# Kernel optimization log

Hardware: AMD Instinct MI355X
Metric: run time of the kernel (lower is better)

Reference implementation:

```python
import jax, jax.numpy as jnp
import numpy as np

B, CHAN, HW = 256, 3, 32
NC, DIM = 10, 48
FC1_IN = (HW - 4) * (HW - 4) * 64 // 4  # 12544


def _signed_root(m, a, p, b):
    # sign(sign(m)+0.1) * ((|m|+a)^p - b)
    return jnp.sign(jnp.sign(m) + 0.1) * (jnp.power(jnp.abs(m) + a, p) - b)


def setup_inputs() -> dict:
    key = jax.random.key(0)
    ks = jax.random.split(key, 12)
    f32 = jnp.float32
    x = jax.random.normal(ks[0], (B, CHAN, HW, HW), f32)
    conv1_w = jax.random.normal(ks[1], (32, CHAN, 3, 3), f32) * (1.0 / np.sqrt(CHAN * 9))
    conv1_b = jax.random.normal(ks[2], (32,), f32) * 0.01
    conv2_w = jax.random.normal(ks[3], (64, 32, 3, 3), f32) * (1.0 / np.sqrt(32 * 9))
    conv2_b = jax.random.normal(ks[4], (64,), f32) * 0.01
    fc1_w = jax.random.normal(ks[5], (128, FC1_IN), f32) * (1.0 / np.sqrt(FC1_IN))
    fc1_b = jax.random.normal(ks[6], (128,), f32) * 0.01
    fc2_w = jax.random.normal(ks[7], (128, 128), f32) * (1.0 / np.sqrt(128))
    fc2_b = jax.random.normal(ks[8], (128,), f32) * 0.01
    fc3_w = jax.random.normal(ks[9], (DIM, 128), f32) * (1.0 / np.sqrt(128))
    fc3_b = jax.random.normal(ks[10], (DIM,), f32) * 0.01
    centers = jnp.eye(NC, DIM, dtype=f32)
    # GaussMoments constants: standard-normal joint moments (non-trainable)
    mom_weight = jnp.ones((DIM,), f32)          # order-1 moment weights, reused for all orders in source
    gm1 = jnp.zeros((DIM,), f32)                # E[z_i] = 0
    eye = jnp.eye(DIM, dtype=f32)
    gm2 = eye                                   # E[z_i z_j] = delta_ij
    gm3 = jnp.zeros((DIM, DIM, DIM), f32)       # odd moments vanish
    gm4 = (eye[:, :, None, None] * eye[None, None, :, :]
           + eye[:, None, :, None] * eye[None, :, None, :]
           + eye[:, None, None, :] * eye[None, :, :, None])  # Isserlis
    return {"x": x, "conv1_w": conv1_w, "conv1_b": conv1_b, "conv2_w": conv2_w,
            "conv2_b": conv2_b, "fc1_w": fc1_w, "fc1_b": fc1_b, "fc2_w": fc2_w,
            "fc2_b": fc2_b, "fc3_w": fc3_w, "fc3_b": fc3_b, "centers": centers,
            "mom_weight": mom_weight, "gm1": gm1, "gm2": gm2, "gm3": gm3, "gm4": gm4}


def _backbone(x, c1w, c1b, c2w, c2b, f1w, f1b, f2w, f2b, f3w, f3b):
    dn = ("NCHW", "OIHW", "NCHW")
    h = jax.lax.conv_general_dilated(x, c1w, (1, 1), "VALID", dimension_numbers=dn)
    h = jax.nn.relu(h + c1b[None, :, None, None])
    h = jax.lax.conv_general_dilated(h, c2w, (1, 1), "VALID", dimension_numbers=dn)
    h = jax.nn.relu(h + c2b[None, :, None, None])
    h = jax.lax.reduce_window(h, -jnp.inf, jax.lax.max, (1, 1, 2, 2), (1, 1, 2, 2), "VALID")
    h = h.reshape(h.shape[0], -1)
    h = jax.nn.relu(h @ f1w.T + f1b)
    h = jax.nn.relu(h @ f2w.T + f2b)
    return h @ f3w.T + f3b  # [B, DIM]


def _gmm_tail(z, centers, mom_weight, gm1, gm2, gm3, gm4):
    Bv, d, C = z.shape[0], DIM, NC
    diff = z[:, None, :] - centers[None, :, :]              # [B,C,d]
    dist_sq = jnp.sum(diff * diff, axis=-1)                 # [B,C]
    expo = -0.5 * dist_sq
    expo_safe = expo - jnp.max(expo, axis=1, keepdims=True)  # MaxPool1d(10) == max over classes
    numer_safe = jnp.exp(expo_safe)
    resp = numer_safe / jnp.sum(numer_safe, axis=1, keepdims=True)
    onehot = jax.nn.one_hot(jnp.argmin(dist_sq, axis=-1), C, dtype=diff.dtype)  # [B,C]
    do = diff * onehot[:, :, None]                          # [B,C,d]
    cw = jnp.sum(onehot, axis=0)                            # [C]
    eps = 1e-7
    m1 = jnp.sum(do, axis=0) / (cw[:, None] + eps)          # [C,d]
    pair = jnp.einsum("bci,bcj->bcij", do, do).reshape(Bv, C, d * d)  # [B,C,d^2]
    m2 = jnp.sum(pair, axis=0).reshape(C, d, d) / (cw[:, None, None] + eps)
    m3 = jnp.einsum("bcp,bck->cpk", pair, do).reshape(C, d, d, d)      # NOT count-normalized (as in source)
    m4 = jnp.einsum("bcp,bcq->cpq", pair, pair).reshape(C, d, d, d, d)  # NOT count-normalized (as in source)
    m2 = _signed_root(m2, 0.25, 0.5, 0.5)
    m3 = _signed_root(m3, 0.19245008973, 0.3333333333, 0.57735026919)
    m4 = _signed_root(m4, 0.15749013123, 0.25, 0.62996052494)
    t1 = gm1
    t2 = _signed_root(gm2, 0.25, 0.5, 0.5)
    t3 = _signed_root(gm3, 0.19245008973, 0.3333333333, 0.57735026919)
    t4 = _signed_root(gm4, 0.15749013123, 0.25, 0.62996052494)
    cwn = cw / jnp.sum(cw)
    # moment weights broadcast over the LAST axis only (torch repeat semantics in source)
    p1 = jnp.sum(cwn[:, None] * mom_weight * (m1 - t1[None]) ** 2)
    p2 = jnp.sum(cwn[:, None, None] * mom_weight * (m2 - t2[None]) ** 2)
    p3 = jnp.sum(cwn[:, None, None, None] * mom_weight * (m3 - t3[None]) ** 2)
    p4 = jnp.sum(cwn[:, None, None, None, None] * mom_weight * (m4 - t4[None]) ** 2)
    log_resp = jnp.log(jnp.clip(resp, 1e-8))
    return log_resp, p1, p2, p3, p4


def reference(x, conv1_w, conv1_b, conv2_w, conv2_b, fc1_w, fc1_b, fc2_w, fc2_b,
              fc3_w, fc3_b, centers, mom_weight, gm1, gm2, gm3, gm4):
    z = _backbone(x, conv1_w, conv1_b, conv2_w, conv2_b, fc1_w, fc1_b, fc2_w, fc2_b, fc3_w, fc3_b)
    return _gmm_tail(z, centers, mom_weight, gm1, gm2, gm3, gm4)
```

## Files before the change

### kernel.cpp

```cpp
#include <hip/hip_runtime.h>
#include <math.h>

#define BATCH   256
#define NCLS    10
#define DIM     48

#define OFF_H1B   0
#define OFF_PAIR  0
#define OFF_FC1P  602112
#define OFF_WT    2699264
#define OFF_PTBH  4500000
#define OFF_PTBL  5300000
#define OFF_POOL  7372800
#define OFF_DO    10596352
#define OFF_CW    10608640
#define OFF_INT   10608656
#define OFF_WPH   10612000
#define OFF_WPL   10622000

typedef __attribute__((ext_vector_type(8))) short short8;
typedef __attribute__((ext_vector_type(4))) float floatx4;
typedef unsigned short u16;
typedef unsigned int u32;

__device__ __forceinline__ u16 f2bf(float v) {
    u32 u = __float_as_uint(v);
    return (u16)((u + 0x7fffu + ((u >> 16) & 1u)) >> 16);
}
__device__ __forceinline__ float bf2f(u16 h) {
    return __uint_as_float(((u32)h) << 16);
}

__device__ __forceinline__ float sroot_half(float m) {
    float s = (m < 0.f) ? -1.f : 1.f;
    return s * (sqrtf(fabsf(m) + 0.25f) - 0.5f);
}
__device__ __forceinline__ float sroot_cbrt(float m) {
    float s = (m < 0.f) ? -1.f : 1.f;
    return s * (cbrtf(fabsf(m) + 0.19245008973f) - 0.57735026919f);
}
__device__ __forceinline__ float sroot_quarter(float m) {
    float s = (m < 0.f) ? -1.f : 1.f;
    return s * (sqrtf(sqrtf(fabsf(m) + 0.15749013123f)) - 0.62996052494f);
}

__global__ void k_conv1(const float* __restrict__ x, const float* __restrict__ w,
                        const float* __restrict__ bias, u16* __restrict__ h1b,
                        const float* __restrict__ c2w, u16* __restrict__ wph,
                        u16* __restrict__ wpl, float* __restrict__ cw,
                        int* __restrict__ cls_cnt, float* __restrict__ out) {
    int blk = blockIdx.x;
    int tid = threadIdx.x;
    if (blk == 900) {
        for (int i = tid; i < 18432; i += 256) {
            int icr = i & 7, rest = i >> 3;
            int oc = rest & 63, rest2 = rest >> 6;
            int icq = rest2 & 3, s = rest2 >> 2;
            int ic = icq * 8 + icr;
            float v = c2w[(oc * 32 + ic) * 9 + s];
            u16 hi = f2bf(v);
            wph[i] = hi;
            wpl[i] = f2bf(v - bf2f(hi));
        }
        return;
    }
    if (blk == 0) {
        if (tid < 16) { cw[tid] = 0.f; cls_cnt[tid] = 0; }
        else if (tid < 20) out[2560 + tid - 16] = 0.f;
    }
    int pos = blk * 256 + tid;
    int b = pos / 900, rem = pos % 900;
    int y = rem / 30, xx = rem % 30;
    float win[27];
#pragma unroll
    for (int ic = 0; ic < 3; ic++)
#pragma unroll
        for (int ky = 0; ky < 3; ky++)
#pragma unroll
            for (int kx = 0; kx < 3; kx++)
                win[ic * 9 + ky * 3 + kx] = x[b * 3072 + ic * 1024 + (y + ky) * 32 + xx + kx];
    u16* hp = h1b + (size_t)pos * 64;
#pragma unroll
    for (int ch = 0; ch < 4; ch++) {
        u32 hiw[4], low[4];
#pragma unroll
        for (int a2 = 0; a2 < 4; a2++) {
            u16 h2[2], l2[2];
#pragma unroll
            for (int e = 0; e < 2; e++) {
                int oc = ch * 8 + a2 * 2 + e;
                float s = bias[oc];
#pragma unroll
                for (int k = 0; k < 27; k++) s = fmaf(win[k], w[oc * 27 + k], s);
                s = fmaxf(s, 0.f);
                u16 hi = f2bf(s);
                h2[e] = hi;
                l2[e] = f2bf(s - bf2f(hi));
            }
            hiw[a2] = (u32)h2[0] | ((u32)h2[1] << 16);
            low[a2] = (u32)l2[0] | ((u32)l2[1] << 16);
        }
        *(uint4*)(hp + ch * 8)      = make_uint4(hiw[0], hiw[1], hiw[2], hiw[3]);
        *(uint4*)(hp + 32 + ch * 8) = make_uint4(low[0], low[1], low[2], low[3]);
    }
}

__global__ void k_conv2(const u16* __restrict__ h1b, const u16* __restrict__ wph,
                        const u16* __restrict__ wpl, const float* __restrict__ bias,
                        float* __restrict__ pooled) {
    __shared__ u16 hs[256 * 72];
    int blk = blockIdx.x;
    int b = blk >> 2, sub = blk & 3;
    int hy = sub >> 1, hx = sub & 1;
    int row0 = hy * 14, col0 = hx * 14;
    int tid = threadIdx.x;
    for (int i = tid; i < 2048; i += 256) {
        int p = i >> 3, c8 = i & 7;
        int r = p >> 4, cc = p & 15;
        size_t gp = (size_t)b * 900 + (size_t)(row0 + r) * 30 + col0 + cc;
        *(uint4*)(&hs[p * 72 + c8 * 8]) = *(const uint4*)(&h1b[gp * 64 + c8 * 8]);
    }
    int wv = tid >> 6, lane = tid & 63;
    int n = lane & 15, quad = lane >> 4;
    int ocb = wv * 16 + n;
    float bv = bias[ocb];
    short8 bh[9], bl[9];
#pragma unroll
    for (int s = 0; s < 9; s++) {
        int off = (((s * 4 + quad) * 64) + ocb) * 8;
        bh[s] = *(const short8*)(&wph[off]);
        bl[s] = *(const short8*)(&wpl[off]);
    }
    __syncthreads();
    int ml = lane & 15;
    for (int t = 0; t < 13; t++) {
        int gA = t * 4 + (ml >> 2);
        int d = ml & 3;
        int gc = (gA < 49) ? gA : 0;
        int py = gc / 7, px = gc % 7;
        int rb = 2 * py + (d >> 1), cb = 2 * px + (d & 1);
        floatx4 acc = {0.f, 0.f, 0.f, 0.f};
#pragma unroll
        for (int s = 0; s < 9; s++) {
            int ky = s / 3, kx = s % 3;
            int pos = (rb + ky) * 16 + cb + kx;
            short8 ah = *(const short8*)(&hs[pos * 72 + quad * 8]);
            short8 al = *(const short8*)(&hs[pos * 72 + 32 + quad * 8]);
            acc = __builtin_amdgcn_mfma_f32_16x16x32_bf16(ah, bh[s], acc, 0, 0, 0);
            acc = __builtin_amdgcn_mfma_f32_16x16x32_bf16(ah, bl[s], acc, 0, 0, 0);
            acc = __builtin_amdgcn_mfma_f32_16x16x32_bf16(al, bh[s], acc, 0, 0, 0);
        }
        int G = t * 4 + quad;
        if (G < 49) {
            float v = fmaxf(fmaxf(acc.x, acc.y), fmaxf(acc.z, acc.w));
            v = fmaxf(v + bv, 0.f);
            int pyg = hy * 7 + G / 7, pxg = hx * 7 + G % 7;
            pooled[(size_t)b * 12544 + ocb * 196 + pyg * 14 + pxg] = v;
        }
    }
}

__global__ void k_wtrans(const float* __restrict__ w, float* __restrict__ wT) {
    __shared__ float tile[32][33];
    int kb = blockIdx.x % 392, nb = blockIdx.x / 392;
    int tid = threadIdx.x;
    int tx = tid & 31, ty = tid >> 5;
    int k0 = kb * 32, n0 = nb * 32;
#pragma unroll
    for (int r = 0; r < 4; r++)
        tile[tx][ty * 4 + r] = w[(n0 + ty * 4 + r) * 12544 + k0 + tx];
    __syncthreads();
#pragma unroll
    for (int r = 0; r < 4; r++)
        wT[(k0 + ty * 4 + r) * 128 + n0 + tx] = tile[ty * 4 + r][tx];
}

__global__ void k_fc1(const float* __restrict__ pooled, const float* __restrict__ wT,
                      float* __restrict__ fc1p) {
    __shared__ __align__(16) float Alds[16 * 196];
    int blk = blockIdx.x;
    int sg = blk >> 6, kc = blk & 63;
    int tid = threadIdx.x;
    int m0 = sg * 16, k0 = kc * 196;
    for (int i = tid; i < 784; i += 256) {
        int m = i / 49, u = i % 49;
        ((float4*)Alds)[m * 49 + u] = ((const float4*)(pooled + (m0 + m) * 12544 + k0))[u];
    }
    __syncthreads();
    int n2 = tid & 63, mg = tid >> 6;
    const float* wp = wT + (size_t)k0 * 128 + n2;
    const float* arow = Alds + mg * 4 * 196;
    float acc[4][2];
#pragma unroll
    for (int j = 0; j < 4; j++) { acc[j][0] = 0.f; acc[j][1] = 0.f; }
    for (int k = 0; k < 196; k += 2) {
        float wa0 = wp[k * 128],        wb0 = wp[k * 128 + 64];
        float wa1 = wp[(k + 1) * 128],  wb1 = wp[(k + 1) * 128 + 64];
#pragma unroll
        for (int j = 0; j < 4; j++) {
            float2 av = *(const float2*)(arow + j * 196 + k);
            acc[j][0] = fmaf(av.x, wa0, acc[j][0]);
            acc[j][0] = fmaf(av.y, wa1, acc[j][0]);
            acc[j][1] = fmaf(av.x, wb0, acc[j][1]);
            acc[j][1] = fmaf(av.y, wb1, acc[j][1]);
        }
    }
#pragma unroll
    for (int j = 0; j < 4; j++) {
        int m = m0 + mg * 4 + j;
        fc1p[kc * 32768 + m * 128 + n2]      = acc[j][0];
        fc1p[kc * 32768 + m * 128 + n2 + 64] = acc[j][1];
    }
}

__global__ void k_fc23a(const float* __restrict__ fc1p, const float* __restrict__ f1b,
                        const float* __restrict__ w2, const float* __restrict__ b2,
                        const float* __restrict__ w3, const float* __restrict__ b3,
                        const float* __restrict__ centers, float* __restrict__ out,
                        float* __restrict__ dov, float* __restrict__ pairm,
                        float* __restrict__ cw, int* __restrict__ cls_cnt,
                        int* __restrict__ cls_idx) {
    __shared__ float a[128], h[128], zb[48], dvs[48];
    __shared__ float dist[10];
    __shared__ float smn, ssum;
    __shared__ int sarg;
    int b = blockIdx.x, t = threadIdx.x;
    float s0 = f1b[t];
    for (int p = 0; p < 64; p++) s0 += fc1p[p * 32768 + b * 128 + t];
    a[t] = fmaxf(s0, 0.f);
    __syncthreads();
    float s = b2[t];
    const float* wr = w2 + t * 128;
#pragma unroll 4
    for (int k = 0; k < 128; k++) s = fmaf(wr[k], a[k], s);
    h[t] = fmaxf(s, 0.f);
    __syncthreads();
    if (t < 48) {
        float s3 = b3[t];
        const float* wr3 = w3 + t * 128;
#pragma unroll 4
        for (int k = 0; k < 128; k++) s3 = fmaf(wr3[k], h[k], s3);
        zb[t] = s3;
    }
    __syncthreads();
    if (t < 10) {
        float d = 0.f;
        const float* cc = centers + t * 48;
        for (int k = 0; k < 48; k++) { float df = zb[k] - cc[k]; d = fmaf(df, df, d); }
        dist[t] = d;
    }
    __syncthreads();
    if (t == 0) {
        float mn = dist[0]; int arg = 0;
        for (int c = 1; c < 10; c++) if (dist[c] < mn) { mn = dist[c]; arg = c; }
        float sum = 0.f;
        for (int c = 0; c < 10; c++) sum += expf(-0.5f * (dist[c] - mn));
        smn = mn; ssum = sum; sarg = arg;
        atomicAdd(&cw[arg], 1.f);
        int pos = atomicAdd(&cls_cnt[arg], 1);
        cls_idx[arg * 256 + pos] = b;
    }
    __syncthreads();
    if (t < 10) {
        float es = -0.5f * (dist[t] - smn);
        float resp = expf(es) / ssum;
        out[b * 10 + t] = logf(fmaxf(resp, 1e-8f));
    }
    if (t < 48) {
        float v = zb[t] - centers[sarg * 48 + t];
        dvs[t] = v;
        dov[b * 48 + t] = v;
    }
    __syncthreads();
#pragma unroll
    for (int e = 0; e < 18; e++) {
        int cell = t + 128 * e;
        pairm[b * 2304 + cell] = dvs[cell / 48] * dvs[cell % 48];
    }
}

__global__ void k_ptrans(const float* __restrict__ pairm, const int* __restrict__ cls_cnt,
                         const int* __restrict__ cls_idx, u16* __restrict__ ptbh,
                         u16* __restrict__ ptbl) {
    __shared__ float tile[32][65];
    __shared__ int cmap[32];
    int blk = blockIdx.x;
    int ctile = blk / 18, coltile = blk % 18;
    int cell0 = ctile * 64, col0 = coltile * 32;
    int tid = threadIdx.x;
    if (tid < 32) {
        int j = col0 + tid;
        int base = 0, samp = -1;
        for (int c = 0; c < 10; c++) {
            int cnt = cls_cnt[c];
            if (j >= base && j < base + cnt) samp = cls_idx[c * 256 + (j - base)];
            base += (cnt + 31) & ~31;
        }
        cmap[tid] = samp;
    }
    __syncthreads();
    for (int i = tid; i < 2048; i += 256) {
        int u = i >> 6, ce = i & 63;
        int s = cmap[u];
        tile[u][ce] = (s >= 0) ? pairm[(size_t)s * 2304 + cell0 + ce] : 0.f;
    }
    __syncthreads();
    for (int i = tid; i < 2048; i += 256) {
        int r = i >> 5, u = i & 31;
        float v = tile[u][r];
        u16 hi = f2bf(v);
        size_t off = (size_t)(cell0 + r) * 576 + col0 + u;
        ptbh[off] = hi;
        ptbl[off] = f2bf(v - bf2f(hi));
    }
}

__global__ void k_tail(const float* __restrict__ pairm, const float* __restrict__ dov,
                       const u16* __restrict__ ptbh, const u16* __restrict__ ptbl,
                       const float* __restrict__ cw, const int* __restrict__ cls_cnt,
                       const int* __restrict__ cls_idx, const float* __restrict__ momw,
                       const float* __restrict__ gm1, const float* __restrict__ gm2,
                       const float* __restrict__ gm3, float* __restrict__ out) {
    __shared__ __align__(16) float smem[12800];
    int blk = blockIdx.x;
    int t = threadIdx.x;

    if (blk < 1710) {
        u16* Ah = (u16*)smem;
        u16* Al = Ah + 5120;
        u16* Bh = Al + 5120;
        u16* Bl = Bh + 5120;
        float* red = smem + 10240;
        int c = blk / 171;
        int cnt = cls_cnt[c];
        if (cnt == 0) return;
        int rem = blk % 171;
        int pt = 0;
        while (rem >= 18 - pt) { rem -= 18 - pt; pt++; }
        int qt = pt + rem;
        int base = 0;
        for (int cc2 = 0; cc2 < c; cc2++) base += (cls_cnt[cc2] + 31) & ~31;
        int kch = (cnt + 31) >> 5;
        int w = t >> 6, lane = t & 63, ml = lane & 15, quad = lane >> 4;
        floatx4 acc[16];
#pragma unroll
        for (int i = 0; i < 16; i++) acc[i] = (floatx4){0.f, 0.f, 0.f, 0.f};
        for (int kc = 0; kc < kch; kc++) {
            __syncthreads();
            for (int i = t; i < 256; i += 256) {
                int row = i & 127, half = i >> 7;
                int grow = (half ? qt : pt) * 128 + row;
                const u16* srch = ptbh + (size_t)grow * 576 + base + kc * 32;
                const u16* srcl = ptbl + (size_t)grow * 576 + base + kc * 32;
                u16* dsth = (half ? Bh : Ah) + row * 40;
                u16* dstl = (half ? Bl : Al) + row * 40;
#pragma unroll
                for (int u2 = 0; u2 < 4; u2++) {
                    *(uint4*)(dsth + u2 * 8) = *(const uint4*)(srch + u2 * 8);
                    *(uint4*)(dstl + u2 * 8) = *(const uint4*)(srcl + u2 * 8);
                }
            }
            __syncthreads();
            short8 ah[2], al[2];
#pragma unroll
            for (int ms = 0; ms < 2; ms++) {
                int ar = (w * 32 + ms * 16 + ml) * 40 + quad * 8;
                ah[ms] = *(const short8*)(Ah + ar);
                al[ms] = *(const short8*)(Al + ar);
            }
#pragma unroll
            for (int ns = 0; ns < 8; ns++) {
                int br = (ns * 16 + ml) * 40 + quad * 8;
                short8 bhv = *(const short8*)(Bh + br);
                short8 blv = *(const short8*)(Bl + br);
#pragma unroll
                for (int ms = 0; ms < 2; ms++) {
                    int id = ms * 8 + ns;
                    acc[id] = __builtin_amdgcn_mfma_f32_16x16x32_bf16(ah[ms], bhv, acc[id], 0, 0, 0);
                    acc[id] = __builtin_amdgcn_mfma_f32_16x16x32_bf16(ah[ms], blv, acc[id], 0, 0, 0);
                    acc[id] = __builtin_amdgcn_mfma_f32_16x16x32_bf16(al[ms], bhv, acc[id], 0, 0, 0);
                }
            }
        }
        float T1 = sroot_quarter(1.f), T3 = sroot_quarter(3.f);
        float cwn = cw[c] * (1.f / 256.f);
        bool diag = (pt == qt);
        float p4c = 0.f;
#pragma unroll
        for (int ns = 0; ns < 8; ns++) {
            int q = qt * 128 + ns * 16 + ml;
            int kq = q / 48, lq = q % 48;
            float mq = momw[lq];
#pragma unroll
            for (int ms = 0; ms < 2; ms++) {
                int id = ms * 8 + ns;
#pragma unroll
                for (int reg = 0; reg < 4; reg++) {
                    int p = pt * 128 + w * 32 + ms * 16 + quad * 4 + reg;
                    int ip = p / 48, jp = p % 48;
                    int g = ((ip == jp) && (kq == lq))
                          + ((ip == kq) && (jp == lq))
                          + ((ip == lq) && (jp == kq));
                    float t4v = (g == 0) ? 0.f : ((g == 1) ? T1 : T3);
                    float d4 = sroot_quarter(acc[id][reg]) - t4v;
                    float wgt = diag ? mq : (mq + momw[jp]);
                    p4c += wgt * d4 * d4;
                }
            }
        }
        p4c *= cwn;
        red[t] = p4c; __syncthreads();
        for (int off = 128; off > 0; off >>= 1) { if (t < off) red[t] += red[t + off]; __syncthreads(); }
        if (t == 0) atomicAdd(&out[2563], red[0]);

    } else if (blk < 2070) {
        float* Pl = smem;
        float* Dl = smem + 4096;
        float* red = smem + 7168;
        int bb = blk - 1710;
        int c = bb / 36, pt = bb % 36;
        int cnt = cls_cnt[c];
        const int* cidx = cls_idx + c * 256;
        int pl = t >> 2, kq = t & 3;
        float acc[12];
#pragma unroll
        for (int m = 0; m < 12; m++) acc[m] = 0.f;
        for (int s0 = 0; s0 < cnt; s0 += 64) {
            int sc = min(64, cnt - s0);
            __syncthreads();
            for (int i = t; i < sc * 16; i += 256) {
                int row = i >> 4, u = i & 15;
                ((float4*)Pl)[row * 16 + u] =
                    ((const float4*)(pairm + (size_t)cidx[s0 + row] * 2304 + pt * 64))[u];
            }
            for (int i = t; i < sc * 12; i += 256) {
                int row = i / 12, u = i % 12;
                ((float4*)Dl)[row * 12 + u] =
                    ((const float4*)(dov + (size_t)cidx[s0 + row] * 48))[u];
            }
            __syncthreads();
            for (int s = 0; s < sc; s++) {
                float pa = Pl[s * 64 + pl];
                float4 d0 = *(const float4*)&Dl[s * 48 + kq * 12];
                float4 d1 = *(const float4*)&Dl[s * 48 + kq * 12 + 4];
                float4 d2 = *(const float4*)&Dl[s * 48 + kq * 12 + 8];
                acc[0]  = fmaf(pa, d0.x, acc[0]);  acc[1]  = fmaf(pa, d0.y, acc[1]);
                acc[2]  = fmaf(pa, d0.z, acc[2]);  acc[3]  = fmaf(pa, d0.w, acc[3]);
                acc[4]  = fmaf(pa, d1.x, acc[4]);  acc[5]  = fmaf(pa, d1.y, acc[5]);
                acc[6]  = fmaf(pa, d1.z, acc[6]);  acc[7]  = fmaf(pa, d1.w, acc[7]);
                acc[8]  = fmaf(pa, d2.x, acc[8]);  acc[9]  = fmaf(pa, d2.y, acc[9]);
                acc[10] = fmaf(pa, d2.z, acc[10]); acc[11] = fmaf(pa, d2.w, acc[11]);
            }
        }
        float cwn = cw[c] * (1.f / 256.f);
        int p = pt * 64 + pl;
        float p3c = 0.f;
#pragma unroll
        for (int m = 0; m < 12; m++) {
            int k = kq * 12 + m;
            float d3 = sroot_cbrt(acc[m]) - sroot_cbrt(gm3[p * 48 + k]);
            p3c += momw[k] * d3 * d3;
        }
        p3c *= cwn;
        red[t] = p3c; __syncthreads();
        for (int off = 128; off > 0; off >>= 1) { if (t < off) red[t] += red[t + off]; __syncthreads(); }
        if (t == 0) atomicAdd(&out[2562], red[0]);

    } else {
        float* ds = smem;
        float* red = smem + 12288;
        int c = blk - 2070;
        int cnt = cls_cnt[c];
        const int* cidx = cls_idx + c * 256;
        for (int i = t; i < cnt * 48; i += 256)
            ds[i] = dov[(size_t)cidx[i / 48] * 48 + (i % 48)];
        __syncthreads();
        float denom = cw[c] + 1e-7f;
        float cwn = cw[c] * (1.f / 256.f);
        float p2c = 0.f;
        for (int r = 0; r < 9; r++) {
            int cell = t + 256 * r;
            int i = cell / 48, j = cell % 48;
            float acc = 0.f;
            for (int s = 0; s < cnt; s++) acc = fmaf(ds[s * 48 + i], ds[s * 48 + j], acc);
            float m2v = acc / denom;
            float d2 = sroot_half(m2v) - sroot_half(gm2[cell]);
            p2c += cwn * momw[j] * d2 * d2;
        }
        red[t] = p2c; __syncthreads();
        for (int off = 128; off > 0; off >>= 1) { if (t < off) red[t] += red[t + off]; __syncthreads(); }
        if (t == 0) atomicAdd(&out[2561], red[0]);
        if (t < 48) {
            float acc = 0.f;
            for (int s = 0; s < cnt; s++) acc += ds[s * 48 + t];
            float m1v = acc / denom;
            float d1 = m1v - gm1[t];
            atomicAdd(&out[2560], cwn * momw[t] * d1 * d1);
        }
    }
}

extern "C" void kernel_launch(void* const* d_in, const int* in_sizes, int n_in,
                              void* d_out, int out_size, void* d_ws, size_t ws_size,
                              hipStream_t stream) {
    const float* x    = (const float*)d_in[0];
    const float* c1w  = (const float*)d_in[1];
    const float* c1b  = (const float*)d_in[2];
    const float* c2w  = (const float*)d_in[3];
    const float* c2b  = (const float*)d_in[4];
    const float* f1w  = (const float*)d_in[5];
    const float* f1b  = (const float*)d_in[6];
    const float* f2w  = (const float*)d_in[7];
    const float* f2b  = (const float*)d_in[8];
    const float* f3w  = (const float*)d_in[9];
    const float* f3b  = (const float*)d_in[10];
    const float* cen  = (const float*)d_in[11];
    const float* momw = (const float*)d_in[12];
    const float* gm1  = (const float*)d_in[13];
    const float* gm2  = (const float*)d_in[14];
    const float* gm3  = (const float*)d_in[15];

    float* ws      = (float*)d_ws;
    u16*   h1b     = (u16*)(ws + OFF_H1B);
    float* pairm   = ws + OFF_PAIR;
    float* fc1p    = ws + OFF_FC1P;
    float* wT      = ws + OFF_WT;
    u16*   ptbh    = (u16*)(ws + OFF_PTBH);
    u16*   ptbl    = (u16*)(ws + OFF_PTBL);
    float* pooled  = ws + OFF_POOL;
    float* dov     = ws + OFF_DO;
    float* cwp     = ws + OFF_CW;
    int*   iws     = (int*)(ws + OFF_INT);
    int*   cls_cnt = iws;
    int*   cls_idx = iws + 16;
    u16*   wph     = (u16*)(ws + OFF_WPH);
    u16*   wpl     = (u16*)(ws + OFF_WPL);
    float* out     = (float*)d_out;

    k_conv1<<<901, 256, 0, stream>>>(x, c1w, c1b, h1b, c2w, wph, wpl,
                                     cwp, cls_cnt, out);
    k_conv2<<<1024, 256, 0, stream>>>(h1b, wph, wpl, c2b, pooled);
    k_wtrans<<<1568, 256, 0, stream>>>(f1w, wT);
    k_fc1<<<1024, 256, 0, stream>>>(pooled, wT, fc1p);
    k_fc23a<<<256, 128, 0, stream>>>(fc1p, f1b, f2w, f2b, f3w, f3b, cen, out,
                                     dov, pairm, cwp, cls_cnt, cls_idx);
    k_ptrans<<<648, 256, 0, stream>>>(pairm, cls_cnt, cls_idx, ptbh, ptbl);
    k_tail<<<2080, 256, 0, stream>>>(pairm, dov, ptbh, ptbl, cwp, cls_cnt, cls_idx,
                                     momw, gm1, gm2, gm3, out);
}
```

Baseline: 288.9 us.

## Pre-swizzle pair matrix into MFMA fragment layout and drop LDS staging in p4 GEMM

The transpose kernel now writes the bf16 hi/lo pair-moment data directly in per-lane MFMA fragment order. The fourth-moment GEMM then loads operands straight from global memory into registers, with no shared-memory staging or barriers, and runs as its own kernel with launch bounds for higher occupancy. The p1/p2 and p3 work moves into the prep kernel, which overlaps with the transpose, and the p2 block streams samples in chunks to use less shared memory. The trade-offs are more redundant global/L2 loads of the B fragments across waves and a changed kernel split.

```diff
diff --git a/kernel.cpp b/kernel.cpp
--- a/kernel.cpp
+++ b/kernel.cpp
@@ -9,8 +9,8 @@
 #define OFF_PAIR  0
 #define OFF_FC1P  602112
 #define OFF_WT    2699264
-#define OFF_PTBH  4500000
-#define OFF_PTBL  5300000
+#define OFF_PTFH  4500000
+#define OFF_PTFL  5300000
 #define OFF_POOL  7372800
 #define OFF_DO    10596352
 #define OFF_CW    10608640
@@ -279,145 +279,54 @@
     }
 }
 
-__global__ void k_ptrans(const float* __restrict__ pairm, const int* __restrict__ cls_cnt,
-                         const int* __restrict__ cls_idx, u16* __restrict__ ptbh,
-                         u16* __restrict__ ptbl) {
-    __shared__ float tile[32][65];
-    __shared__ int cmap[32];
-    int blk = blockIdx.x;
-    int ctile = blk / 18, coltile = blk % 18;
-    int cell0 = ctile * 64, col0 = coltile * 32;
-    int tid = threadIdx.x;
-    if (tid < 32) {
-        int j = col0 + tid;
-        int base = 0, samp = -1;
-        for (int c = 0; c < 10; c++) {
-            int cnt = cls_cnt[c];
-            if (j >= base && j < base + cnt) samp = cls_idx[c * 256 + (j - base)];
-            base += (cnt + 31) & ~31;
-        }
-        cmap[tid] = samp;
-    }
-    __syncthreads();
-    for (int i = tid; i < 2048; i += 256) {
-        int u = i >> 6, ce = i & 63;
-        int s = cmap[u];
-        tile[u][ce] = (s >= 0) ? pairm[(size_t)s * 2304 + cell0 + ce] : 0.f;
-    }
-    __syncthreads();
-    for (int i = tid; i < 2048; i += 256) {
-        int r = i >> 5, u = i & 31;
-        float v = tile[u][r];
-        u16 hi = f2bf(v);
-        size_t off = (size_t)(cell0 + r) * 576 + col0 + u;
-        ptbh[off] = hi;
-        ptbl[off] = f2bf(v - bf2f(hi));
-    }
-}
-
-__global__ void k_tail(const float* __restrict__ pairm, const float* __restrict__ dov,
-                       const u16* __restrict__ ptbh, const u16* __restrict__ ptbl,
+__global__ void k_prep(const float* __restrict__ pairm, const float* __restrict__ dov,
                        const float* __restrict__ cw, const int* __restrict__ cls_cnt,
                        const int* __restrict__ cls_idx, const float* __restrict__ momw,
                        const float* __restrict__ gm1, const float* __restrict__ gm2,
-                       const float* __restrict__ gm3, float* __restrict__ out) {
-    __shared__ __align__(16) float smem[12800];
+                       const float* __restrict__ gm3, u16* __restrict__ ptfh,
+                       u16* __restrict__ ptfl, float* __restrict__ out) {
+    __shared__ __align__(16) float smem[7424];
     int blk = blockIdx.x;
     int t = threadIdx.x;
 
-    if (blk < 1710) {
-        u16* Ah = (u16*)smem;
-        u16* Al = Ah + 5120;
-        u16* Bh = Al + 5120;
-        u16* Bl = Bh + 5120;
-        float* red = smem + 10240;
-        int c = blk / 171;
-        int cnt = cls_cnt[c];
-        if (cnt == 0) return;
-        int rem = blk % 171;
-        int pt = 0;
-        while (rem >= 18 - pt) { rem -= 18 - pt; pt++; }
-        int qt = pt + rem;
-        int base = 0;
-        for (int cc2 = 0; cc2 < c; cc2++) base += (cls_cnt[cc2] + 31) & ~31;
-        int kch = (cnt + 31) >> 5;
-        int w = t >> 6, lane = t & 63, ml = lane & 15, quad = lane >> 4;
-        floatx4 acc[16];
-#pragma unroll
-        for (int i = 0; i < 16; i++) acc[i] = (floatx4){0.f, 0.f, 0.f, 0.f};
-        for (int kc = 0; kc < kch; kc++) {
-            __syncthreads();
-            for (int i = t; i < 256; i += 256) {
-                int row = i & 127, half = i >> 7;
-                int grow = (half ? qt : pt) * 128 + row;
-                const u16* srch = ptbh + (size_t)grow * 576 + base + kc * 32;
-                const u16* srcl = ptbl + (size_t)grow * 576 + base + kc * 32;
-                u16* dsth = (half ? Bh : Ah) + row * 40;
-                u16* dstl = (half ? Bl : Al) + row * 40;
-#pragma unroll
-                for (int u2 = 0; u2 < 4; u2++) {
-                    *(uint4*)(dsth + u2 * 8) = *(const uint4*)(srch + u2 * 8);
-                    *(uint4*)(dstl + u2 * 8) = *(const uint4*)(srcl + u2 * 8);
-                }
-            }
-            __syncthreads();
-            short8 ah[2], al[2];
-#pragma unroll
-            for (int ms = 0; ms < 2; ms++) {
-                int ar = (w * 32 + ms * 16 + ml) * 40 + quad * 8;
-                ah[ms] = *(const short8*)(Ah + ar);
-                al[ms] = *(const short8*)(Al + ar);
-            }
-#pragma unroll
-            for (int ns = 0; ns < 8; ns++) {
-                int br = (ns * 16 + ml) * 40 + quad * 8;
-                short8 bhv = *(const short8*)(Bh + br);
-                short8 blv = *(const short8*)(Bl + br);
-#pragma unroll
-                for (int ms = 0; ms < 2; ms++) {
-                    int id = ms * 8 + ns;
-                    acc[id] = __builtin_amdgcn_mfma_f32_16x16x32_bf16(ah[ms], bhv, acc[id], 0, 0, 0);
-                    acc[id] = __builtin_amdgcn_mfma_f32_16x16x32_bf16(ah[ms], blv, acc[id], 0, 0, 0);
-                    acc[id] = __builtin_amdgcn_mfma_f32_16x16x32_bf16(al[ms], bhv, acc[id], 0, 0, 0);
-                }
-            }
-        }
-        float T1 = sroot_quarter(1.f), T3 = sroot_quarter(3.f);
-        float cwn = cw[c] * (1.f / 256.f);
-        bool diag = (pt == qt);
-        float p4c = 0.f;
-#pragma unroll
-        for (int ns = 0; ns < 8; ns++) {
-            int q = qt * 128 + ns * 16 + ml;
-            int kq = q / 48, lq = q % 48;
-            float mq = momw[lq];
-#pragma unroll
-            for (int ms = 0; ms < 2; ms++) {
-                int id = ms * 8 + ns;
-#pragma unroll
-                for (int reg = 0; reg < 4; reg++) {
-                    int p = pt * 128 + w * 32 + ms * 16 + quad * 4 + reg;
-                    int ip = p / 48, jp = p % 48;
-                    int g = ((ip == jp) && (kq == lq))
-                          + ((ip == kq) && (jp == lq))
-                          + ((ip == lq) && (jp == kq));
-                    float t4v = (g == 0) ? 0.f : ((g == 1) ? T1 : T3);
-                    float d4 = sroot_quarter(acc[id][reg]) - t4v;
-                    float wgt = diag ? mq : (mq + momw[jp]);
-                    p4c += wgt * d4 * d4;
-                }
-            }
-        }
-        p4c *= cwn;
-        red[t] = p4c; __syncthreads();
-        for (int off = 128; off > 0; off >>= 1) { if (t < off) red[t] += red[t + off]; __syncthreads(); }
-        if (t == 0) atomicAdd(&out[2563], red[0]);
-
-    } else if (blk < 2070) {
+    if (blk < 648) {
+        float* tile = smem;
+        int* cmap = (int*)(smem + 2080);
+        int ctile = blk / 18, coltile = blk % 18;
+        int cell0 = ctile * 64, col0 = coltile * 32;
+        if (t < 32) {
+            int j = col0 + t, base = 0, samp = -1;
+            for (int c = 0; c < 10; c++) {
+                int cnt = cls_cnt[c];
+                if (j >= base && j < base + cnt) samp = cls_idx[c * 256 + (j - base)];
+                base += (cnt + 31) & ~31;
+            }
+            cmap[t] = samp;
+        }
+        __syncthreads();
+        for (int i = t; i < 2048; i += 256) {
+            int u = i >> 6, ce = i & 63;
+            int s = cmap[u];
+            tile[u * 65 + ce] = (s >= 0) ? pairm[(size_t)s * 2304 + cell0 + ce] : 0.f;
+        }
+        __syncthreads();
+        int kc = col0 >> 5;
+        int rt0 = cell0 >> 4;
+        for (int o = t; o < 2048; o += 256) {
+            int rtl = o >> 9, lane = (o >> 3) & 63, j = o & 7;
+            int m = lane & 15, quad = lane >> 4;
+            float v = tile[(quad * 8 + j) * 65 + rtl * 16 + m];
+            u16 hi = f2bf(v);
+            size_t off = ((size_t)((rt0 + rtl) * 18 + kc) * 64 + lane) * 8 + j;
+            ptfh[off] = hi;
+            ptfl[off] = f2bf(v - bf2f(hi));
+        }
+
+    } else if (blk < 1008) {
         float* Pl = smem;
         float* Dl = smem + 4096;
         float* red = smem + 7168;
-        int bb = blk - 1710;
+        int bb = blk - 648;
         int c = bb / 36, pt = bb % 36;
         int cnt = cls_cnt[c];
         const int* cidx = cls_idx + c * 256;
@@ -468,36 +377,140 @@
 
     } else {
         float* ds = smem;
-        float* red = smem + 12288;
-        int c = blk - 2070;
+        float* red = smem + 3072;
+        int c = blk - 1008;
         int cnt = cls_cnt[c];
         const int* cidx = cls_idx + c * 256;
-        for (int i = t; i < cnt * 48; i += 256)
-            ds[i] = dov[(size_t)cidx[i / 48] * 48 + (i % 48)];
-        __syncthreads();
+        float acc9[9];
+#pragma unroll
+        for (int r = 0; r < 9; r++) acc9[r] = 0.f;
+        float m1a = 0.f;
+        for (int s0 = 0; s0 < cnt; s0 += 64) {
+            int sc = min(64, cnt - s0);
+            __syncthreads();
+            for (int i = t; i < sc * 48; i += 256)
+                ds[i] = dov[(size_t)cidx[s0 + i / 48] * 48 + (i % 48)];
+            __syncthreads();
+#pragma unroll
+            for (int r = 0; r < 9; r++) {
+                int cell = t + 256 * r;
+                int i = cell / 48, j = cell % 48;
+                float a = acc9[r];
+                for (int s = 0; s < sc; s++) a = fmaf(ds[s * 48 + i], ds[s * 48 + j], a);
+                acc9[r] = a;
+            }
+            if (t < 48)
+                for (int s = 0; s < sc; s++) m1a += ds[s * 48 + t];
+        }
         float denom = cw[c] + 1e-7f;
         float cwn = cw[c] * (1.f / 256.f);
         float p2c = 0.f;
+#pragma unroll
         for (int r = 0; r < 9; r++) {
             int cell = t + 256 * r;
-            int i = cell / 48, j = cell % 48;
-            float acc = 0.f;
-            for (int s = 0; s < cnt; s++) acc = fmaf(ds[s * 48 + i], ds[s * 48 + j], acc);
-            float m2v = acc / denom;
+            int j = cell % 48;
+            float m2v = acc9[r] / denom;
             float d2 = sroot_half(m2v) - sroot_half(gm2[cell]);
             p2c += cwn * momw[j] * d2 * d2;
         }
+        __syncthreads();
         red[t] = p2c; __syncthreads();
         for (int off = 128; off > 0; off >>= 1) { if (t < off) red[t] += red[t + off]; __syncthreads(); }
         if (t == 0) atomicAdd(&out[2561], red[0]);
         if (t < 48) {
-            float acc = 0.f;
-            for (int s = 0; s < cnt; s++) acc += ds[s * 48 + t];
-            float m1v = acc / denom;
+            float m1v = m1a / denom;
             float d1 = m1v - gm1[t];
             atomicAdd(&out[2560], cwn * momw[t] * d1 * d1);
         }
     }
+}
+
+__global__ __launch_bounds__(256, 4)
+void k_p4(const u16* __restrict__ ptfh, const u16* __restrict__ ptfl,
+          const float* __restrict__ cw, const int* __restrict__ cls_cnt,
+          const float* __restrict__ momw, float* __restrict__ out) {
+    __shared__ float red[256];
+    int blk = blockIdx.x;
+    int c = blk / 171;
+    int cnt = cls_cnt[c];
+    if (cnt == 0) return;
+    int rem = blk % 171;
+    int pt = 0;
+    while (rem >= 18 - pt) { rem -= 18 - pt; pt++; }
+    int qt = pt + rem;
+    int kc0 = 0;
+    for (int cc = 0; cc < c; cc++) kc0 += (cls_cnt[cc] + 31) >> 5;
+    int kch = (cnt + 31) >> 5;
+    int t = threadIdx.x;
+    int w = t >> 6, lane = t & 63;
+    int ml = lane & 15, quad = lane >> 4;
+    floatx4 acc[16];
+#pragma unroll
+    for (int i = 0; i < 16; i++) acc[i] = (floatx4){0.f, 0.f, 0.f, 0.f};
+    for (int kc = 0; kc < kch; kc++) {
+        short8 ah[2], al[2];
+#pragma unroll
+        for (int ms = 0; ms < 2; ms++) {
+            int art = pt * 8 + w * 2 + ms;
+            size_t aoff = ((size_t)(art * 18 + kc0 + kc) * 64 + lane) * 8;
+            ah[ms] = *(const short8*)(ptfh + aoff);
+            al[ms] = *(const short8*)(ptfl + aoff);
+        }
+#pragma unroll
+        for (int ns = 0; ns < 8; ns++) {
+            int brt = qt * 8 + ns;
+            size_t boff = ((size_t)(brt * 18 + kc0 + kc) * 64 + lane) * 8;
+            short8 bhv = *(const short8*)(ptfh + boff);
+            short8 blv = *(const short8*)(ptfl + boff);
+#pragma unroll
+            for (int ms = 0; ms < 2; ms++) {
+                int id = ms * 8 + ns;
+                acc[id] = __builtin_amdgcn_mfma_f32_16x16x32_bf16(ah[ms], bhv, acc[id], 0, 0, 0);
+                acc[id] = __builtin_amdgcn_mfma_f32_16x16x32_bf16(ah[ms], blv, acc[id], 0, 0, 0);
+                acc[id] = __builtin_amdgcn_mfma_f32_16x16x32_bf16(al[ms], bhv, acc[id], 0, 0, 0);
+            }
+        }
+    }
+    float T1 = sroot_quarter(1.f), T3 = sroot_quarter(3.f);
+    float cwn = cw[c] * (1.f / 256.f);
+    bool diag = (pt == qt);
+    int ipv[8], jpv[8];
+    float mwpv[8];
+#pragma unroll
+    for (int ms = 0; ms < 2; ms++)
+#pragma unroll
+        for (int reg = 0; reg < 4; reg++) {
+            int p = (pt * 8 + w * 2 + ms) * 16 + quad * 4 + reg;
+            ipv[ms * 4 + reg] = p / 48;
+            jpv[ms * 4 + reg] = p % 48;
+            mwpv[ms * 4 + reg] = momw[p % 48];
+        }
+    float p4c = 0.f;
+#pragma unroll
+    for (int ns = 0; ns < 8; ns++) {
+        int q = (qt * 8 + ns) * 16 + ml;
+        int kq = q / 48, lq = q % 48;
+        float mq = momw[lq];
+#pragma unroll
+        for (int ms = 0; ms < 2; ms++) {
+            int id = ms * 8 + ns;
+#pragma unroll
+            for (int reg = 0; reg < 4; reg++) {
+                int ip = ipv[ms * 4 + reg], jp = jpv[ms * 4 + reg];
+                int g = ((ip == jp) && (kq == lq))
+                      + ((ip == kq) && (jp == lq))
+                      + ((ip == lq) && (jp == kq));
+                float t4v = (g == 0) ? 0.f : ((g == 1) ? T1 : T3);
+                float d4 = sroot_quarter(acc[id][reg]) - t4v;
+                float wgt = diag ? mq : (mq + mwpv[ms * 4 + reg]);
+                p4c += wgt * d4 * d4;
+            }
+        }
+    }
+    p4c *= cwn;
+    red[t] = p4c; __syncthreads();
+    for (int off = 128; off > 0; off >>= 1) { if (t < off) red[t] += red[t + off]; __syncthreads(); }
+    if (t == 0) atomicAdd(&out[2563], red[0]);
 }
 
 extern "C" void kernel_launch(void* const* d_in, const int* in_sizes, int n_in,
@@ -525,8 +538,8 @@
     float* pairm   = ws + OFF_PAIR;
     float* fc1p    = ws + OFF_FC1P;
     float* wT      = ws + OFF_WT;
-    u16*   ptbh    = (u16*)(ws + OFF_PTBH);
-    u16*   ptbl    = (u16*)(ws + OFF_PTBL);
+    u16*   ptfh    = (u16*)(ws + OFF_PTFH);
+    u16*   ptfl    = (u16*)(ws + OFF_PTFL);
     float* pooled  = ws + OFF_POOL;
     float* dov     = ws + OFF_DO;
     float* cwp     = ws + OFF_CW;
@@ -544,7 +557,7 @@
     k_fc1<<<1024, 256, 0, stream>>>(pooled, wT, fc1p);
     k_fc23a<<<256, 128, 0, stream>>>(fc1p, f1b, f2w, f2b, f3w, f3b, cen, out,
                                      dov, pairm, cwp, cls_cnt, cls_idx);
-    k_ptrans<<<648, 256, 0, stream>>>(pairm, cls_cnt, cls_idx, ptbh, ptbl);
-    k_tail<<<2080, 256, 0, stream>>>(pairm, dov, ptbh, ptbl, cwp, cls_cnt, cls_idx,
-                                     momw, gm1, gm2, gm3, out);
-}
+    k_prep<<<1018, 256, 0, stream>>>(pairm, dov, cwp, cls_cnt, cls_idx, momw,
+                                     gm1, gm2, gm3, ptfh, ptfl, out);
+    k_p4<<<1710, 256, 0, stream>>>(ptfh, ptfl, cwp, cls_cnt, momw, out);
+}
```

Measured after the change: 273.4 us. -5.4%, faster.
